# Optimization experiments

Hardware: AMD Instinct MI355X
Metric: run time of the kernel (lower is better)

## Reference

```python
import jax, jax.numpy as jnp
import numpy as np

N = 100000   # nodes
E = 1200000  # edges
D = 64       # in_dim = out_dim, heads=1


def setup_inputs() -> dict:
    key = jax.random.key(0)
    ks = jax.random.split(key, 10)
    s = 1.0 / np.sqrt(D)
    return {
        "x": jax.random.normal(ks[0], (N, D), dtype=jnp.float32),
        "edge_index": jax.random.randint(ks[1], (2, E), 0, N, dtype=jnp.int64),
        "Wq": jax.random.uniform(ks[2], (D, D), jnp.float32, -s, s),
        "bq": jnp.zeros((D,), jnp.float32),
        "Wk": jax.random.uniform(ks[3], (D, D), jnp.float32, -s, s),
        "bk": jnp.zeros((D,), jnp.float32),
        "Wv": jax.random.uniform(ks[4], (D, D), jnp.float32, -s, s),
        "bv": jnp.zeros((D,), jnp.float32),
        "Ws": jax.random.uniform(ks[5], (D, D), jnp.float32, -s, s),
        "bs": jnp.zeros((D,), jnp.float32),
    }


def reference(x, edge_index, Wq, bq, Wk, bk, Wv, bv, Ws, bs):
    # TransformerConv (heads=1, concat=True, root_weight=True) + ReLU.
    # Dropout is identity (eval mode).
    src = edge_index[0]  # message source j
    dst = edge_index[1]  # message target i (aggregation segment)

    q = x @ Wq + bq  # [N, D] query of target nodes
    k = x @ Wk + bk  # [N, D] key of source nodes
    v = x @ Wv + bv  # [N, D] value of source nodes

    # per-edge attention logits: (q_i . k_j) / sqrt(D)
    scores = jnp.sum(q[dst] * k[src], axis=-1) * (1.0 / np.sqrt(D))  # [E]

    # segment softmax over incoming edges of each target node
    seg_max = jax.ops.segment_max(scores, dst, num_segments=N)  # [N]
    ex = jnp.exp(scores - seg_max[dst])                          # [E]
    denom = jax.ops.segment_sum(ex, dst, num_segments=N)         # [N]
    alpha = ex / denom[dst]                                      # [E]

    # attention-weighted aggregation of values, then skip connection
    agg = jax.ops.segment_sum(alpha[:, None] * v[src], dst, num_segments=N)  # [N, D]
    h = agg + (x @ Ws + bs)
    return jax.nn.relu(h)
```

## Files before the change

### kernel.cpp

```cpp
#include <hip/hip_runtime.h>

#define D 64
#define NBMAX 256
#define CAP 8192
#define TILE 4096

typedef __attribute__((ext_vector_type(8))) short bf16x8;
typedef __attribute__((ext_vector_type(4))) float f32x4;

__device__ __forceinline__ unsigned f2bfu(float f) {
    unsigned u = __float_as_uint(f);
    return (u + 0x7fffu + ((u >> 16) & 1u)) >> 16;
}
__device__ __forceinline__ short f2bf(float f) { return (short)f2bfu(f); }

__global__ void k_prep(const float* __restrict__ Wq, const float* __restrict__ bq,
                       const float* __restrict__ Wk, const float* __restrict__ bk,
                       const float* __restrict__ Wv, const float* __restrict__ bv,
                       const float* __restrict__ Ws, const float* __restrict__ bs,
                       short* __restrict__ WcT, float* __restrict__ bcat,
                       int* __restrict__ tail, int NB) {
    int gtid = blockIdx.x * 256 + threadIdx.x;
    if (gtid < 256 * D) {
        int c = gtid >> 6, kk = gtid & 63;
        int m = c >> 6;
        const float* W = (m == 0) ? Wq : (m == 1) ? Wk : (m == 2) ? Wv : Ws;
        WcT[c * D + kk] = f2bf(W[kk * D + (c & 63)]);
        if (kk == 0) {
            const float* b = (m == 0) ? bq : (m == 1) ? bk : (m == 2) ? bv : bs;
            bcat[c] = b[c & 63];
        }
    }
    if (gtid < NB) tail[gtid] = gtid * CAP;
}

__global__ void k_binA(const int* __restrict__ src, const int* __restrict__ dst,
                       int* __restrict__ tail, unsigned* __restrict__ binned, int E) {
    __shared__ unsigned s_ent[TILE];
    __shared__ unsigned short s_bkt[TILE];
    __shared__ unsigned s_sorted[TILE];
    __shared__ unsigned short s_bks[TILE];
    __shared__ int hist[NBMAX];
    __shared__ int lo[NBMAX];
    __shared__ int gbase[NBMAX];
    __shared__ int sm[NBMAX];
    int tid = threadIdx.x;
    int ntiles = (E + TILE - 1) / TILE;
    for (int tix = blockIdx.x; tix < ntiles; tix += gridDim.x) {
        int t0 = tix * TILE;
        int n = min(TILE, E - t0);
        if (tid < NBMAX) hist[tid] = 0;
        __syncthreads();
        for (int i = tid; i < n; i += 512) {
            int s = src[t0 + i], d = dst[t0 + i];
            int b = d >> 9;
            s_ent[i] = ((unsigned)s << 9) | (unsigned)(d & 511);
            s_bkt[i] = (unsigned short)b;
            atomicAdd(&hist[b], 1);
        }
        __syncthreads();
        int hv = 0;
        if (tid < NBMAX) { hv = hist[tid]; sm[tid] = hv; }
        __syncthreads();
#pragma unroll
        for (int off = 1; off < NBMAX; off <<= 1) {
            int t = (tid >= off && tid < NBMAX) ? sm[tid - off] : 0;
            __syncthreads();
            if (tid < NBMAX) sm[tid] += t;
            __syncthreads();
        }
        if (tid < NBMAX) {
            lo[tid] = sm[tid] - hv;
            if (hv > 0) gbase[tid] = atomicAdd(&tail[tid], hv);
            hist[tid] = 0;
        }
        __syncthreads();
        for (int i = tid; i < n; i += 512) {
            int b = s_bkt[i];
            int idx = atomicAdd(&hist[b], 1);
            int slot = lo[b] + idx;
            s_sorted[slot] = s_ent[i];
            s_bks[slot] = (unsigned short)b;
        }
        __syncthreads();
        for (int i = tid; i < n; i += 512) {
            int b = s_bks[i];
            binned[gbase[b] + (i - lo[b])] = s_sorted[i];
        }
        __syncthreads();
    }
}

__global__ void k_fat(const unsigned* __restrict__ binned, const int* __restrict__ tail,
                      int* __restrict__ srcs, int* __restrict__ start,
                      int* __restrict__ cnt, int NB,
                      const float* __restrict__ x, const short* __restrict__ WcT,
                      const float* __restrict__ bcat, float* __restrict__ q,
                      unsigned* __restrict__ kvh, float* __restrict__ outp, int N) {
    __shared__ int hist[512];
    __shared__ int lo[512];
    __shared__ int sm[256];
    int tid = threadIdx.x;

    if ((int)blockIdx.x < NB) {
        int b = blockIdx.x;
        int e0 = b * CAP, e1 = tail[b];
        int node0 = b << 9;
        hist[tid] = 0; hist[tid + 256] = 0;
        __syncthreads();
        for (int i = e0 + tid; i < e1; i += 256)
            atomicAdd(&hist[binned[i] & 511], 1);
        __syncthreads();
        int v0 = hist[2 * tid], v1 = hist[2 * tid + 1];
        int ps = v0 + v1;
        sm[tid] = ps;
        __syncthreads();
#pragma unroll
        for (int off = 1; off < 256; off <<= 1) {
            int t = (tid >= off) ? sm[tid - off] : 0;
            __syncthreads();
            sm[tid] += t;
            __syncthreads();
        }
        int excl = sm[tid] - ps;
        lo[2 * tid] = excl;
        lo[2 * tid + 1] = excl + v0;
        int n0 = node0 + 2 * tid;
        if (n0 < N)     { start[n0] = e0 + excl;          cnt[n0] = v0; }
        if (n0 + 1 < N) { start[n0 + 1] = e0 + excl + v0; cnt[n0 + 1] = v1; }
        hist[tid] = 0; hist[tid + 256] = 0;
        __syncthreads();
        for (int i = e0 + tid; i < e1; i += 256) {
            unsigned ent = binned[i];
            int dl = ent & 511;
            int idx = atomicAdd(&hist[dl], 1);
            srcs[e0 + lo[dl] + idx] = (int)(ent >> 9);
        }
        return;
    }

    int bid = (int)blockIdx.x - NB;
    int lane = tid & 63;
    int w = tid >> 6;
    int trow = bid * 64 + w * 16;
    int arow = trow + (lane & 15);
    int kbase = (lane >> 4) * 8;

    bf16x8 a0, a1;
    if (arow < N) {
        const float* xr = x + (size_t)arow * D;
        float4 f0 = *(const float4*)(xr + kbase);
        float4 f1 = *(const float4*)(xr + kbase + 4);
        float4 f2 = *(const float4*)(xr + 32 + kbase);
        float4 f3 = *(const float4*)(xr + 32 + kbase + 4);
        a0 = (bf16x8){f2bf(f0.x), f2bf(f0.y), f2bf(f0.z), f2bf(f0.w),
                      f2bf(f1.x), f2bf(f1.y), f2bf(f1.z), f2bf(f1.w)};
        a1 = (bf16x8){f2bf(f2.x), f2bf(f2.y), f2bf(f2.z), f2bf(f2.w),
                      f2bf(f3.x), f2bf(f3.y), f2bf(f3.z), f2bf(f3.w)};
    } else {
        a0 = (bf16x8){0, 0, 0, 0, 0, 0, 0, 0};
        a1 = (bf16x8){0, 0, 0, 0, 0, 0, 0, 0};
    }

    int l15 = lane & 15;
    int rbase = trow + ((lane >> 4) << 2);

#pragma unroll
    for (int g = 0; g < 2; ++g) {
        int ctbase = (g == 0) ? 0 : 12;
        float* dstp = (g == 0) ? q : outp;
#pragma unroll
        for (int j = 0; j < 4; ++j) {
            int col = (ctbase + j) * 16 + l15;
            const short* wr = WcT + col * D + kbase;
            bf16x8 b0 = *(const bf16x8*)(wr);
            bf16x8 b1 = *(const bf16x8*)(wr + 32);
            f32x4 acc = {0.f, 0.f, 0.f, 0.f};
            acc = __builtin_amdgcn_mfma_f32_16x16x32_bf16(a0, b0, acc, 0, 0, 0);
            acc = __builtin_amdgcn_mfma_f32_16x16x32_bf16(a1, b1, acc, 0, 0, 0);
            float bias = bcat[col];
            int cmod = col & 63;
#pragma unroll
            for (int r = 0; r < 4; ++r) {
                int row = rbase + r;
                if (row < N) dstp[(size_t)row * D + cmod] = acc[r] + bias;
            }
        }
    }
#pragma unroll
    for (int j = 0; j < 4; ++j) {
        int kcol = (4 + j) * 16 + l15;
        int vcol = (8 + j) * 16 + l15;
        const short* wrk = WcT + kcol * D + kbase;
        const short* wrv = WcT + vcol * D + kbase;
        bf16x8 bk0 = *(const bf16x8*)(wrk);
        bf16x8 bk1 = *(const bf16x8*)(wrk + 32);
        bf16x8 bv0 = *(const bf16x8*)(wrv);
        bf16x8 bv1 = *(const bf16x8*)(wrv + 32);
        f32x4 ak = {0.f, 0.f, 0.f, 0.f}, av = {0.f, 0.f, 0.f, 0.f};
        ak = __builtin_amdgcn_mfma_f32_16x16x32_bf16(a0, bk0, ak, 0, 0, 0);
        ak = __builtin_amdgcn_mfma_f32_16x16x32_bf16(a1, bk1, ak, 0, 0, 0);
        av = __builtin_amdgcn_mfma_f32_16x16x32_bf16(a0, bv0, av, 0, 0, 0);
        av = __builtin_amdgcn_mfma_f32_16x16x32_bf16(a1, bv1, av, 0, 0, 0);
        float biask = bcat[kcol], biasv = bcat[vcol];
        int cmod = kcol & 63;
#pragma unroll
        for (int r = 0; r < 4; ++r) {
            int row = rbase + r;
            if (row < N) {
                unsigned kb = f2bfu(ak[r] + biask);
                unsigned vb = f2bfu(av[r] + biasv);
                kvh[(size_t)row * D + cmod] = kb | (vb << 16);
            }
        }
    }
}

__global__ void k_fused(const int* __restrict__ srcs, const int* __restrict__ start,
                        const int* __restrict__ cnt,
                        const float* __restrict__ q, const unsigned* __restrict__ kvh,
                        float* __restrict__ out, int N) {
    int wid = (int)((blockIdx.x * (size_t)blockDim.x + threadIdx.x) >> 6);
    int lane = threadIdx.x & 63;
    if (wid >= N) return;
    int g = lane >> 4, j = lane & 15;
    int s0 = start[wid];
    int c  = cnt[wid];
    int s1 = s0 + c;
    size_t qo = (size_t)wid * D + j * 4;
    float4 qv = *(const float4*)(q + qo);
    qv.x *= 0.125f; qv.y *= 0.125f; qv.z *= 0.125f; qv.w *= 0.125f;
    float a0 = 0.f, a1 = 0.f, a2 = 0.f, a3 = 0.f, l = 0.f;
    for (int t = s0; t < s1; t += 16) {
        int eA = t + g, eB = t + 4 + g, eC = t + 8 + g, eD = t + 12 + g;
        int iA = min(eA, s1 - 1), iB = min(eB, s1 - 1);
        int iC = min(eC, s1 - 1), iD = min(eD, s1 - 1);
        int sjA = srcs[iA], sjB = srcs[iB], sjC = srcs[iC], sjD = srcs[iD];
        uint4 uA = *(const uint4*)(kvh + (size_t)sjA * D + j * 4);
        uint4 uB = *(const uint4*)(kvh + (size_t)sjB * D + j * 4);
        uint4 uC = *(const uint4*)(kvh + (size_t)sjC * D + j * 4);
        uint4 uD = *(const uint4*)(kvh + (size_t)sjD * D + j * 4);
        float pA, pB, pC, pD;
        pA = __uint_as_float(uA.x << 16) * qv.x;
        pA = fmaf(__uint_as_float(uA.y << 16), qv.y, pA);
        pA = fmaf(__uint_as_float(uA.z << 16), qv.z, pA);
        pA = fmaf(__uint_as_float(uA.w << 16), qv.w, pA);
        pB = __uint_as_float(uB.x << 16) * qv.x;
        pB = fmaf(__uint_as_float(uB.y << 16), qv.y, pB);
        pB = fmaf(__uint_as_float(uB.z << 16), qv.z, pB);
        pB = fmaf(__uint_as_float(uB.w << 16), qv.w, pB);
        pC = __uint_as_float(uC.x << 16) * qv.x;
        pC = fmaf(__uint_as_float(uC.y << 16), qv.y, pC);
        pC = fmaf(__uint_as_float(uC.z << 16), qv.z, pC);
        pC = fmaf(__uint_as_float(uC.w << 16), qv.w, pC);
        pD = __uint_as_float(uD.x << 16) * qv.x;
        pD = fmaf(__uint_as_float(uD.y << 16), qv.y, pD);
        pD = fmaf(__uint_as_float(uD.z << 16), qv.z, pD);
        pD = fmaf(__uint_as_float(uD.w << 16), qv.w, pD);
#pragma unroll
        for (int off = 1; off < 16; off <<= 1) {
            pA += __shfl_xor(pA, off, 64);
            pB += __shfl_xor(pB, off, 64);
            pC += __shfl_xor(pC, off, 64);
            pD += __shfl_xor(pD, off, 64);
        }
        float eAf = (eA < s1) ? __expf(pA) : 0.f;
        float eBf = (eB < s1) ? __expf(pB) : 0.f;
        float eCf = (eC < s1) ? __expf(pC) : 0.f;
        float eDf = (eD < s1) ? __expf(pD) : 0.f;
        l += (eAf + eBf) + (eCf + eDf);
        a0 = fmaf(eAf, __uint_as_float(uA.x & 0xffff0000u), a0);
        a1 = fmaf(eAf, __uint_as_float(uA.y & 0xffff0000u), a1);
        a2 = fmaf(eAf, __uint_as_float(uA.z & 0xffff0000u), a2);
        a3 = fmaf(eAf, __uint_as_float(uA.w & 0xffff0000u), a3);
        a0 = fmaf(eBf, __uint_as_float(uB.x & 0xffff0000u), a0);
        a1 = fmaf(eBf, __uint_as_float(uB.y & 0xffff0000u), a1);
        a2 = fmaf(eBf, __uint_as_float(uB.z & 0xffff0000u), a2);
        a3 = fmaf(eBf, __uint_as_float(uB.w & 0xffff0000u), a3);
        a0 = fmaf(eCf, __uint_as_float(uC.x & 0xffff0000u), a0);
        a1 = fmaf(eCf, __uint_as_float(uC.y & 0xffff0000u), a1);
        a2 = fmaf(eCf, __uint_as_float(uC.z & 0xffff0000u), a2);
        a3 = fmaf(eCf, __uint_as_float(uC.w & 0xffff0000u), a3);
        a0 = fmaf(eDf, __uint_as_float(uD.x & 0xffff0000u), a0);
        a1 = fmaf(eDf, __uint_as_float(uD.y & 0xffff0000u), a1);
        a2 = fmaf(eDf, __uint_as_float(uD.z & 0xffff0000u), a2);
        a3 = fmaf(eDf, __uint_as_float(uD.w & 0xffff0000u), a3);
    }
#pragma unroll
    for (int off = 16; off < 64; off <<= 1) {
        a0 += __shfl_xor(a0, off, 64);
        a1 += __shfl_xor(a1, off, 64);
        a2 += __shfl_xor(a2, off, 64);
        a3 += __shfl_xor(a3, off, 64);
        l  += __shfl_xor(l,  off, 64);
    }
    if (g == 0) {
        float inv = (c > 0) ? 1.f / l : 0.f;
        float4 sk = *(const float4*)(out + qo);
        float4 r;
        r.x = fmaxf(fmaf(a0, inv, sk.x), 0.f);
        r.y = fmaxf(fmaf(a1, inv, sk.y), 0.f);
        r.z = fmaxf(fmaf(a2, inv, sk.z), 0.f);
        r.w = fmaxf(fmaf(a3, inv, sk.w), 0.f);
        *(float4*)(out + qo) = r;
    }
}

extern "C" void kernel_launch(void* const* d_in, const int* in_sizes, int n_in,
                              void* d_out, int out_size, void* d_ws, size_t ws_size,
                              hipStream_t stream) {
    const float* x  = (const float*)d_in[0];
    const int*   ei = (const int*)d_in[1];
    const float* Wq = (const float*)d_in[2]; const float* bq = (const float*)d_in[3];
    const float* Wk = (const float*)d_in[4]; const float* bk = (const float*)d_in[5];
    const float* Wv = (const float*)d_in[6]; const float* bv = (const float*)d_in[7];
    const float* Ws = (const float*)d_in[8]; const float* bs = (const float*)d_in[9];

    int N = in_sizes[0] / D;
    int E = in_sizes[1] / 2;
    const int* src = ei;
    const int* dst = ei + E;
    float* out = (float*)d_out;

    int NB = (N + 511) >> 9;

    float*    q      = (float*)d_ws;
    unsigned* kvh    = (unsigned*)(q + (size_t)N * D);
    unsigned* binned = kvh + (size_t)N * D;
    int*      srcs   = (int*)(binned + (size_t)NB * CAP);
    int*      start  = srcs + (size_t)NB * CAP;
    int*      cnt    = start + N;
    int*      tail   = cnt + N;
    short*    WcT    = (short*)(tail + NBMAX);
    float*    bcat   = (float*)(WcT + 256 * D);

    k_prep<<<64, 256, 0, stream>>>(Wq, bq, Wk, bk, Wv, bv, Ws, bs,
                                   WcT, bcat, tail, NB);
    int ntiles = (E + TILE - 1) / TILE;
    k_binA<<<(ntiles < 512 ? ntiles : 512), 512, 0, stream>>>(src, dst, tail, binned, E);
    int mb = (N + 63) / 64;
    k_fat<<<NB + mb, 256, 0, stream>>>(binned, tail, srcs, start, cnt, NB,
                                       x, WcT, bcat, q, kvh, out, N);
    k_fused<<<(N + 3) / 4, 256, 0, stream>>>(srcs, start, cnt, q, kvh, out, N);
}
```

Before: 116.8 us.

## Merge weight prep into binning kernel and simplify edge binning to direct scatter

Folds the weight transpose/bf16 conversion into the binning kernel as extra blocks, which removes one kernel launch, and replaces the per-bucket tail initialization with a hipMemsetAsync of counters. The binning step drops the shared-memory local sort and prefix scan. Each block now takes one chunk, builds a histogram, reserves global space with atomics and scatters entries directly, so stores are less coalesced but the LDS work and synchronizations go away. Order within a bucket becomes nondeterministic, which the downstream per-bucket counting sort should tolerate.

```diff
diff --git a/kernel.cpp b/kernel.cpp
--- a/kernel.cpp
+++ b/kernel.cpp
@@ -3,7 +3,8 @@
 #define D 64
 #define NBMAX 256
 #define CAP 8192
-#define TILE 4096
+#define CHUNK 4096
+#define PREPB 64
 
 typedef __attribute__((ext_vector_type(8))) short bf16x8;
 typedef __attribute__((ext_vector_type(4))) float f32x4;
@@ -14,14 +15,16 @@
 }
 __device__ __forceinline__ short f2bf(float f) { return (short)f2bfu(f); }
 
-__global__ void k_prep(const float* __restrict__ Wq, const float* __restrict__ bq,
+__global__ void k_binA(const float* __restrict__ Wq, const float* __restrict__ bq,
                        const float* __restrict__ Wk, const float* __restrict__ bk,
                        const float* __restrict__ Wv, const float* __restrict__ bv,
                        const float* __restrict__ Ws, const float* __restrict__ bs,
                        short* __restrict__ WcT, float* __restrict__ bcat,
-                       int* __restrict__ tail, int NB) {
-    int gtid = blockIdx.x * 256 + threadIdx.x;
-    if (gtid < 256 * D) {
+                       const int* __restrict__ src, const int* __restrict__ dst,
+                       int* __restrict__ tailcnt, unsigned* __restrict__ binned, int E) {
+    int tid = threadIdx.x;
+    if ((int)blockIdx.x < PREPB) {
+        int gtid = blockIdx.x * 256 + tid;
         int c = gtid >> 6, kk = gtid & 63;
         int m = c >> 6;
         const float* W = (m == 0) ? Wq : (m == 1) ? Wk : (m == 2) ? Wv : Ws;
@@ -30,68 +33,33 @@
             const float* b = (m == 0) ? bq : (m == 1) ? bk : (m == 2) ? bv : bs;
             bcat[c] = b[c & 63];
         }
-    }
-    if (gtid < NB) tail[gtid] = gtid * CAP;
-}
-
-__global__ void k_binA(const int* __restrict__ src, const int* __restrict__ dst,
-                       int* __restrict__ tail, unsigned* __restrict__ binned, int E) {
-    __shared__ unsigned s_ent[TILE];
-    __shared__ unsigned short s_bkt[TILE];
-    __shared__ unsigned s_sorted[TILE];
-    __shared__ unsigned short s_bks[TILE];
+        return;
+    }
     __shared__ int hist[NBMAX];
-    __shared__ int lo[NBMAX];
     __shared__ int gbase[NBMAX];
-    __shared__ int sm[NBMAX];
-    int tid = threadIdx.x;
-    int ntiles = (E + TILE - 1) / TILE;
-    for (int tix = blockIdx.x; tix < ntiles; tix += gridDim.x) {
-        int t0 = tix * TILE;
-        int n = min(TILE, E - t0);
-        if (tid < NBMAX) hist[tid] = 0;
-        __syncthreads();
-        for (int i = tid; i < n; i += 512) {
-            int s = src[t0 + i], d = dst[t0 + i];
-            int b = d >> 9;
-            s_ent[i] = ((unsigned)s << 9) | (unsigned)(d & 511);
-            s_bkt[i] = (unsigned short)b;
-            atomicAdd(&hist[b], 1);
-        }
-        __syncthreads();
-        int hv = 0;
-        if (tid < NBMAX) { hv = hist[tid]; sm[tid] = hv; }
-        __syncthreads();
-#pragma unroll
-        for (int off = 1; off < NBMAX; off <<= 1) {
-            int t = (tid >= off && tid < NBMAX) ? sm[tid - off] : 0;
-            __syncthreads();
-            if (tid < NBMAX) sm[tid] += t;
-            __syncthreads();
-        }
-        if (tid < NBMAX) {
-            lo[tid] = sm[tid] - hv;
-            if (hv > 0) gbase[tid] = atomicAdd(&tail[tid], hv);
-            hist[tid] = 0;
-        }
-        __syncthreads();
-        for (int i = tid; i < n; i += 512) {
-            int b = s_bkt[i];
-            int idx = atomicAdd(&hist[b], 1);
-            int slot = lo[b] + idx;
-            s_sorted[slot] = s_ent[i];
-            s_bks[slot] = (unsigned short)b;
-        }
-        __syncthreads();
-        for (int i = tid; i < n; i += 512) {
-            int b = s_bks[i];
-            binned[gbase[b] + (i - lo[b])] = s_sorted[i];
-        }
-        __syncthreads();
-    }
-}
-
-__global__ void k_fat(const unsigned* __restrict__ binned, const int* __restrict__ tail,
+    int cid = (int)blockIdx.x - PREPB;
+    int t0 = cid * CHUNK;
+    int n = min(CHUNK, E - t0);
+    if (tid < NBMAX) hist[tid] = 0;
+    __syncthreads();
+    for (int i = tid; i < n; i += 256)
+        atomicAdd(&hist[dst[t0 + i] >> 9], 1);
+    __syncthreads();
+    if (tid < NBMAX) {
+        int hv = hist[tid];
+        gbase[tid] = (hv > 0) ? (tid * CAP + atomicAdd(&tailcnt[tid], hv)) : 0;
+        hist[tid] = 0;
+    }
+    __syncthreads();
+    for (int i = tid; i < n; i += 256) {
+        int s = src[t0 + i], d = dst[t0 + i];
+        int b = d >> 9;
+        int idx = atomicAdd(&hist[b], 1);
+        binned[gbase[b] + idx] = ((unsigned)s << 9) | (unsigned)(d & 511);
+    }
+}
+
+__global__ void k_fat(const unsigned* __restrict__ binned, const int* __restrict__ tailcnt,
                       int* __restrict__ srcs, int* __restrict__ start,
                       int* __restrict__ cnt, int NB,
                       const float* __restrict__ x, const short* __restrict__ WcT,
@@ -104,7 +72,7 @@
 
     if ((int)blockIdx.x < NB) {
         int b = blockIdx.x;
-        int e0 = b * CAP, e1 = tail[b];
+        int e0 = b * CAP, e1 = e0 + tailcnt[b];
         int node0 = b << 9;
         hist[tid] = 0; hist[tid + 256] = 0;
         __syncthreads();
@@ -330,16 +298,17 @@
     int*      srcs   = (int*)(binned + (size_t)NB * CAP);
     int*      start  = srcs + (size_t)NB * CAP;
     int*      cnt    = start + N;
-    int*      tail   = cnt + N;
-    short*    WcT    = (short*)(tail + NBMAX);
+    int*      tailcnt= cnt + N;
+    short*    WcT    = (short*)(tailcnt + NBMAX);
     float*    bcat   = (float*)(WcT + 256 * D);
 
-    k_prep<<<64, 256, 0, stream>>>(Wq, bq, Wk, bk, Wv, bv, Ws, bs,
-                                   WcT, bcat, tail, NB);
-    int ntiles = (E + TILE - 1) / TILE;
-    k_binA<<<(ntiles < 512 ? ntiles : 512), 512, 0, stream>>>(src, dst, tail, binned, E);
+    hipMemsetAsync(tailcnt, 0, NBMAX * sizeof(int), stream);
+
+    int nchunks = (E + CHUNK - 1) / CHUNK;
+    k_binA<<<PREPB + nchunks, 256, 0, stream>>>(Wq, bq, Wk, bk, Wv, bv, Ws, bs,
+                                                WcT, bcat, src, dst, tailcnt, binned, E);
     int mb = (N + 63) / 64;
-    k_fat<<<NB + mb, 256, 0, stream>>>(binned, tail, srcs, start, cnt, NB,
+    k_fat<<<NB + mb, 256, 0, stream>>>(binned, tailcnt, srcs, start, cnt, NB,
                                        x, WcT, bcat, q, kvh, out, N);
     k_fused<<<(N + 3) / 4, 256, 0, stream>>>(srcs, start, cnt, q, kvh, out, N);
 }
```

Measured after the change: 124.0 us. 6.2% more time.

## Merge weight prep into binning kernel and widen fat kernel to 512 threads

Applied to the files above, without the earlier changes.

Folds the weight-transpose/bias prep into extra blocks of the binning kernel and replaces the tail initialization with a memset plus relative counters, removing one kernel launch. Binning now uses one block per tile instead of a grid-stride loop. The CSR-building/GEMM kernel moves to 512 threads per block, with one node per thread in the scan and 128 rows per GEMM block. This cuts launch count and serial dependencies, at the cost of a memset call and changed occupancy.

```diff
diff --git a/kernel.cpp b/kernel.cpp
--- a/kernel.cpp
+++ b/kernel.cpp
@@ -4,6 +4,7 @@
 #define NBMAX 256
 #define CAP 8192
 #define TILE 4096
+#define PREPB 32
 
 typedef __attribute__((ext_vector_type(8))) short bf16x8;
 typedef __attribute__((ext_vector_type(4))) float f32x4;
@@ -14,14 +15,16 @@
 }
 __device__ __forceinline__ short f2bf(float f) { return (short)f2bfu(f); }
 
-__global__ void k_prep(const float* __restrict__ Wq, const float* __restrict__ bq,
+__global__ void k_binA(const float* __restrict__ Wq, const float* __restrict__ bq,
                        const float* __restrict__ Wk, const float* __restrict__ bk,
                        const float* __restrict__ Wv, const float* __restrict__ bv,
                        const float* __restrict__ Ws, const float* __restrict__ bs,
                        short* __restrict__ WcT, float* __restrict__ bcat,
-                       int* __restrict__ tail, int NB) {
-    int gtid = blockIdx.x * 256 + threadIdx.x;
-    if (gtid < 256 * D) {
+                       const int* __restrict__ src, const int* __restrict__ dst,
+                       int* __restrict__ tailcnt, unsigned* __restrict__ binned, int E) {
+    int tid = threadIdx.x;
+    if ((int)blockIdx.x < PREPB) {
+        int gtid = blockIdx.x * 512 + tid;
         int c = gtid >> 6, kk = gtid & 63;
         int m = c >> 6;
         const float* W = (m == 0) ? Wq : (m == 1) ? Wk : (m == 2) ? Wv : Ws;
@@ -30,12 +33,8 @@
             const float* b = (m == 0) ? bq : (m == 1) ? bk : (m == 2) ? bv : bs;
             bcat[c] = b[c & 63];
         }
-    }
-    if (gtid < NB) tail[gtid] = gtid * CAP;
-}
-
-__global__ void k_binA(const int* __restrict__ src, const int* __restrict__ dst,
-                       int* __restrict__ tail, unsigned* __restrict__ binned, int E) {
+        return;
+    }
     __shared__ unsigned s_ent[TILE];
     __shared__ unsigned short s_bkt[TILE];
     __shared__ unsigned s_sorted[TILE];
@@ -44,54 +43,49 @@
     __shared__ int lo[NBMAX];
     __shared__ int gbase[NBMAX];
     __shared__ int sm[NBMAX];
-    int tid = threadIdx.x;
-    int ntiles = (E + TILE - 1) / TILE;
-    for (int tix = blockIdx.x; tix < ntiles; tix += gridDim.x) {
-        int t0 = tix * TILE;
-        int n = min(TILE, E - t0);
-        if (tid < NBMAX) hist[tid] = 0;
-        __syncthreads();
-        for (int i = tid; i < n; i += 512) {
-            int s = src[t0 + i], d = dst[t0 + i];
-            int b = d >> 9;
-            s_ent[i] = ((unsigned)s << 9) | (unsigned)(d & 511);
-            s_bkt[i] = (unsigned short)b;
-            atomicAdd(&hist[b], 1);
-        }
-        __syncthreads();
-        int hv = 0;
-        if (tid < NBMAX) { hv = hist[tid]; sm[tid] = hv; }
-        __syncthreads();
-#pragma unroll
-        for (int off = 1; off < NBMAX; off <<= 1) {
-            int t = (tid >= off && tid < NBMAX) ? sm[tid - off] : 0;
-            __syncthreads();
-            if (tid < NBMAX) sm[tid] += t;
-            __syncthreads();
-        }
-        if (tid < NBMAX) {
-            lo[tid] = sm[tid] - hv;
-            if (hv > 0) gbase[tid] = atomicAdd(&tail[tid], hv);
-            hist[tid] = 0;
-        }
-        __syncthreads();
-        for (int i = tid; i < n; i += 512) {
-            int b = s_bkt[i];
-            int idx = atomicAdd(&hist[b], 1);
-            int slot = lo[b] + idx;
-            s_sorted[slot] = s_ent[i];
-            s_bks[slot] = (unsigned short)b;
-        }
-        __syncthreads();
-        for (int i = tid; i < n; i += 512) {
-            int b = s_bks[i];
-            binned[gbase[b] + (i - lo[b])] = s_sorted[i];
-        }
-        __syncthreads();
-    }
-}
-
-__global__ void k_fat(const unsigned* __restrict__ binned, const int* __restrict__ tail,
+    int t0 = ((int)blockIdx.x - PREPB) * TILE;
+    int n = min(TILE, E - t0);
+    if (tid < NBMAX) hist[tid] = 0;
+    __syncthreads();
+    for (int i = tid; i < n; i += 512) {
+        int s = src[t0 + i], d = dst[t0 + i];
+        int b = d >> 9;
+        s_ent[i] = ((unsigned)s << 9) | (unsigned)(d & 511);
+        s_bkt[i] = (unsigned short)b;
+        atomicAdd(&hist[b], 1);
+    }
+    __syncthreads();
+    int hv = 0;
+    if (tid < NBMAX) { hv = hist[tid]; sm[tid] = hv; }
+    __syncthreads();
+#pragma unroll
+    for (int off = 1; off < NBMAX; off <<= 1) {
+        int t = (tid >= off && tid < NBMAX) ? sm[tid - off] : 0;
+        __syncthreads();
+        if (tid < NBMAX) sm[tid] += t;
+        __syncthreads();
+    }
+    if (tid < NBMAX) {
+        lo[tid] = sm[tid] - hv;
+        if (hv > 0) gbase[tid] = tid * CAP + atomicAdd(&tailcnt[tid], hv);
+        hist[tid] = 0;
+    }
+    __syncthreads();
+    for (int i = tid; i < n; i += 512) {
+        int b = s_bkt[i];
+        int idx = atomicAdd(&hist[b], 1);
+        int slot = lo[b] + idx;
+        s_sorted[slot] = s_ent[i];
+        s_bks[slot] = (unsigned short)b;
+    }
+    __syncthreads();
+    for (int i = tid; i < n; i += 512) {
+        int b = s_bks[i];
+        binned[gbase[b] + (i - lo[b])] = s_sorted[i];
+    }
+}
+
+__global__ void k_fat(const unsigned* __restrict__ binned, const int* __restrict__ tailcnt,
                       int* __restrict__ srcs, int* __restrict__ start,
                       int* __restrict__ cnt, int NB,
                       const float* __restrict__ x, const short* __restrict__ WcT,
@@ -99,38 +93,34 @@
                       unsigned* __restrict__ kvh, float* __restrict__ outp, int N) {
     __shared__ int hist[512];
     __shared__ int lo[512];
-    __shared__ int sm[256];
+    __shared__ int sm[512];
     int tid = threadIdx.x;
 
     if ((int)blockIdx.x < NB) {
         int b = blockIdx.x;
-        int e0 = b * CAP, e1 = tail[b];
-        int node0 = b << 9;
-        hist[tid] = 0; hist[tid + 256] = 0;
-        __syncthreads();
-        for (int i = e0 + tid; i < e1; i += 256)
+        int e0 = b * CAP, e1 = e0 + tailcnt[b];
+        hist[tid] = 0;
+        __syncthreads();
+        for (int i = e0 + tid; i < e1; i += 512)
             atomicAdd(&hist[binned[i] & 511], 1);
         __syncthreads();
-        int v0 = hist[2 * tid], v1 = hist[2 * tid + 1];
-        int ps = v0 + v1;
-        sm[tid] = ps;
-        __syncthreads();
-#pragma unroll
-        for (int off = 1; off < 256; off <<= 1) {
+        int v = hist[tid];
+        sm[tid] = v;
+        __syncthreads();
+#pragma unroll
+        for (int off = 1; off < 512; off <<= 1) {
             int t = (tid >= off) ? sm[tid - off] : 0;
             __syncthreads();
             sm[tid] += t;
             __syncthreads();
         }
-        int excl = sm[tid] - ps;
-        lo[2 * tid] = excl;
-        lo[2 * tid + 1] = excl + v0;
-        int n0 = node0 + 2 * tid;
-        if (n0 < N)     { start[n0] = e0 + excl;          cnt[n0] = v0; }
-        if (n0 + 1 < N) { start[n0 + 1] = e0 + excl + v0; cnt[n0 + 1] = v1; }
-        hist[tid] = 0; hist[tid + 256] = 0;
-        __syncthreads();
-        for (int i = e0 + tid; i < e1; i += 256) {
+        int excl = sm[tid] - v;
+        lo[tid] = excl;
+        int node = (b << 9) + tid;
+        if (node < N) { start[node] = e0 + excl; cnt[node] = v; }
+        hist[tid] = 0;
+        __syncthreads();
+        for (int i = e0 + tid; i < e1; i += 512) {
             unsigned ent = binned[i];
             int dl = ent & 511;
             int idx = atomicAdd(&hist[dl], 1);
@@ -142,7 +132,7 @@
     int bid = (int)blockIdx.x - NB;
     int lane = tid & 63;
     int w = tid >> 6;
-    int trow = bid * 64 + w * 16;
+    int trow = bid * 128 + w * 16;
     int arow = trow + (lane & 15);
     int kbase = (lane >> 4) * 8;
 
@@ -330,16 +320,17 @@
     int*      srcs   = (int*)(binned + (size_t)NB * CAP);
     int*      start  = srcs + (size_t)NB * CAP;
     int*      cnt    = start + N;
-    int*      tail   = cnt + N;
-    short*    WcT    = (short*)(tail + NBMAX);
+    int*      tailcnt= cnt + N;
+    short*    WcT    = (short*)(tailcnt + NBMAX);
     float*    bcat   = (float*)(WcT + 256 * D);
 
-    k_prep<<<64, 256, 0, stream>>>(Wq, bq, Wk, bk, Wv, bv, Ws, bs,
-                                   WcT, bcat, tail, NB);
+    hipMemsetAsync(tailcnt, 0, NBMAX * sizeof(int), stream);
+
     int ntiles = (E + TILE - 1) / TILE;
-    k_binA<<<(ntiles < 512 ? ntiles : 512), 512, 0, stream>>>(src, dst, tail, binned, E);
-    int mb = (N + 63) / 64;
-    k_fat<<<NB + mb, 256, 0, stream>>>(binned, tail, srcs, start, cnt, NB,
+    k_binA<<<PREPB + ntiles, 512, 0, stream>>>(Wq, bq, Wk, bk, Wv, bv, Ws, bs,
+                                               WcT, bcat, src, dst, tailcnt, binned, E);
+    int mb = (N + 127) / 128;
+    k_fat<<<NB + mb, 512, 0, stream>>>(binned, tailcnt, srcs, start, cnt, NB,
                                        x, WcT, bcat, q, kvh, out, N);
     k_fused<<<(N + 3) / 4, 256, 0, stream>>>(srcs, start, cnt, q, kvh, out, N);
 }
```

Measured after the change: 119.6 us. +2.3%, slower.
